# Optimization experiments

Measured on AMD Instinct MI355X. Metric: run time of the kernel, lower is better.

Reference implementation:

```python
import jax, jax.numpy as jnp
from jax import lax
import numpy as np

DIM = 768
HEADS = 12
HD = DIM // HEADS  # 64
STRIDE = (1, 2, 2)
KER = (3, 3, 3)
PAD = [(1, 1), (1, 1), (1, 1)]
EPS = 1e-5


def _layernorm(x, g, b):
    mu = jnp.mean(x, axis=-1, keepdims=True)
    var = jnp.var(x, axis=-1, keepdims=True)
    return (x - mu) * lax.rsqrt(var + EPS) * g + b


def _attention_pool(t, wconv, g, b, T, H, W):
    # t: [B, heads, 1 + T*H*W, HD]; depthwise conv3d pooling on non-cls tokens
    B, Nh, _, Cd = t.shape
    cls_tok = t[:, :, :1, :]
    body = t[:, :, 1:, :].reshape(B * Nh, T, H, W, Cd).transpose(0, 4, 1, 2, 3)  # [BN, C, T, H, W]
    body = lax.conv_general_dilated(
        body, wconv, window_strides=STRIDE, padding=PAD,
        feature_group_count=Cd,
        dimension_numbers=('NCDHW', 'OIDHW', 'NCDHW'))
    Tp, Hp, Wp = body.shape[2], body.shape[3], body.shape[4]
    body = body.reshape(B, Nh, Cd, Tp * Hp * Wp).transpose(0, 1, 3, 2)  # [B, heads, Lp, C]
    t = jnp.concatenate([cls_tok, body], axis=2)
    t = _layernorm(t, g, b)
    return t, (Tp, Hp, Wp)


def setup_inputs() -> dict:
    key = jax.random.key(0)
    ks = jax.random.split(key, 12)
    T, H, W = 8, 28, 28
    B = 4
    N = 1 + T * H * W  # cls + thw tokens = 6273
    s = 0.02
    inp = {
        'x': jax.random.normal(ks[0], (B, N, DIM), jnp.float32),
        'qkv_w': jax.random.normal(ks[1], (DIM, 3 * DIM), jnp.float32) * s,
        'qkv_b': jnp.zeros((3 * DIM,), jnp.float32),
        'proj_w': jax.random.normal(ks[2], (DIM, DIM), jnp.float32) * s,
        'proj_b': jnp.zeros((DIM,), jnp.float32),
        'wq': jax.random.normal(ks[3], (HD, 1, 3, 3, 3), jnp.float32) * s,
        'wk': jax.random.normal(ks[4], (HD, 1, 3, 3, 3), jnp.float32) * s,
        'wv': jax.random.normal(ks[5], (HD, 1, 3, 3, 3), jnp.float32) * s,
        'gq': jnp.ones((HD,), jnp.float32), 'bq': jnp.zeros((HD,), jnp.float32),
        'gk': jnp.ones((HD,), jnp.float32), 'bk': jnp.zeros((HD,), jnp.float32),
        'gv': jnp.ones((HD,), jnp.float32), 'bv': jnp.zeros((HD,), jnp.float32),
        'thw_t': T, 'thw_h': H, 'thw_w': W,
    }
    return inp


def reference(x, qkv_w, qkv_b, proj_w, proj_b, wq, wk, wv,
              gq, bq, gk, bk, gv, bv, thw_t, thw_h, thw_w):
    B, N, C = x.shape
    scale = HD ** -0.5
    qkv = (x @ qkv_w + qkv_b).reshape(B, N, 3, HEADS, HD).transpose(2, 0, 3, 1, 4)
    q, k, v = qkv[0], qkv[1], qkv[2]  # [B, heads, N, HD]
    q, q_shape = _attention_pool(q, wq, gq, bq, thw_t, thw_h, thw_w)
    k, _ = _attention_pool(k, wk, gk, bk, thw_t, thw_h, thw_w)
    v, _ = _attention_pool(v, wv, gv, bv, thw_t, thw_h, thw_w)
    attn = jax.nn.softmax(jnp.einsum('bhqd,bhkd->bhqk', q, k) * scale, axis=-1)
    Nq = q.shape[2]
    out = jnp.einsum('bhqk,bhkd->bhqd', attn, v).transpose(0, 2, 1, 3).reshape(B, Nq, C)
    out = out @ proj_w + proj_b
    return out
```

## Files before the change

kernel.cpp:

```cpp
#include <hip/hip_runtime.h>
#include <hip/hip_bf16.h>

#define BB      4
#define NTOK    6273
#define NPOOL   1569
#define NPOOLP  1600
#define NHEADS  12
#define TT      8
#define HH      28
#define WW      28
#define HP      14
#define WP      14

typedef __attribute__((ext_vector_type(8))) _Float16 f16x8;
typedef __attribute__((ext_vector_type(4))) float f32x4;
typedef unsigned short u16;

#define AS1(p) ((const __attribute__((address_space(1))) void*)(p))
#define AS3(p) ((__attribute__((address_space(3))) void*)(p))

static __device__ __forceinline__ u16 f2h(float x) {
    union { _Float16 h; u16 u; } c; c.h = (_Float16)x; return c.u;
}
static __device__ __forceinline__ float h2f(u16 u) {
    union { u16 u; _Float16 h; } c; c.u = u; return (float)c.h;
}

__global__ __launch_bounds__(256) void cvt_f32_f16_kernel(
    const float* __restrict__ in, u16* __restrict__ out, int n4)
{
    int i = blockIdx.x * 256 + threadIdx.x;
    const int stride = gridDim.x * 256;
    for (; i < n4; i += stride) {
        const float4 v = ((const float4*)in)[i];
        ushort4 o;
        o.x = f2h(v.x); o.y = f2h(v.y); o.z = f2h(v.z); o.w = f2h(v.w);
        ((ushort4*)out)[i] = o;
    }
}

__global__ __launch_bounds__(256) void transpose_cvt_kernel(
    const float* __restrict__ W, u16* __restrict__ t, int K, int N)
{
    __shared__ float tile[32][33];
    const int n0 = blockIdx.x * 32, k0 = blockIdx.y * 32;
    const int tx = threadIdx.x, ty = threadIdx.y;
    #pragma unroll
    for (int i = 0; i < 4; ++i)
        tile[ty + i * 8][tx] = W[(size_t)(k0 + ty + i * 8) * N + n0 + tx];
    __syncthreads();
    #pragma unroll
    for (int i = 0; i < 4; ++i) {
        const int n = n0 + ty + i * 8;
        t[(size_t)n * K + k0 + tx] = f2h(tile[tx][ty + i * 8]);
    }
}

__global__ __launch_bounds__(256) void wt_transpose_kernel(
    const float* __restrict__ wq, const float* __restrict__ wk,
    const float* __restrict__ wv, u16* __restrict__ wTh)
{
    const int which = blockIdx.x;
    const float* w = (which == 0) ? wq : (which == 1) ? wk : wv;
    u16* o = wTh + which * 27 * 64;
    for (int i = threadIdx.x; i < 27 * 64; i += 256) {
        const int j = i >> 6, d = i & 63;
        o[j * 64 + d] = f2h(w[d * 27 + j]);
    }
}

#define GBK 32
#define GNKT 24

__global__ __launch_bounds__(512, 2) void gemm256_qkv_kernel(
    const u16* __restrict__ Af, const u16* __restrict__ Bt,
    const float* __restrict__ bias, int M,
    u16* __restrict__ o0, u16* __restrict__ o1, u16* __restrict__ o2)
{
    __shared__ __align__(16) u16 AB_s[3][2][256 * GBK];

    const int tid  = threadIdx.x;
    const int lane = tid & 63;
    const int w    = tid >> 6;
    const int wr   = w >> 2, wc = w & 3;

    const int nwg = gridDim.x;
    const int qch = nwg >> 3, rch = nwg & 7;
    const int xcd = blockIdx.x & 7, idx = blockIdx.x >> 3;
    const int wg  = (xcd < rch ? xcd * (qch + 1) : rch * (qch + 1) + (xcd - rch) * qch) + idx;
    const int m0 = (wg / 9) * 256;
    const int nb = wg % 9;
    const int n0 = nb * 256;

    const int ch0 = tid, ch1 = 512 + tid;
    const int r0 = ch0 >> 2, c0 = ((ch0 & 3) ^ (r0 & 3)) << 3;
    const int r1 = ch1 >> 2, c1 = ((ch1 & 3) ^ (r1 & 3)) << 3;
    const u16* pA0 = Af + (size_t)min(m0 + r0, M - 1) * 768 + c0;
    const u16* pA1 = Af + (size_t)min(m0 + r1, M - 1) * 768 + c1;
    const u16* pB0 = Bt + (size_t)(n0 + r0) * 768 + c0;
    const u16* pB1 = Bt + (size_t)(n0 + r1) * 768 + c1;
    const int dst0 = (w * 64) * 8;
    const int dst1 = (512 + w * 64) * 8;

    #define STAGE_A(buf, kk) do { \
        __builtin_amdgcn_global_load_lds(AS1(pA0 + (kk)), AS3(&AB_s[buf][0][dst0]), 16, 0, 0); \
        __builtin_amdgcn_global_load_lds(AS1(pA1 + (kk)), AS3(&AB_s[buf][0][dst1]), 16, 0, 0); \
    } while (0)
    #define STAGE_B(buf, kk) do { \
        __builtin_amdgcn_global_load_lds(AS1(pB0 + (kk)), AS3(&AB_s[buf][1][dst0]), 16, 0, 0); \
        __builtin_amdgcn_global_load_lds(AS1(pB1 + (kk)), AS3(&AB_s[buf][1][dst1]), 16, 0, 0); \
    } while (0)

    STAGE_A(0, 0);  STAGE_B(0, 0);
    STAGE_A(1, GBK); STAGE_B(1, GBK);

    f32x4 acc[8][4] = {};
    const int fr = lane & 15, fq = lane >> 4;
    const int sw8 = (fq ^ (fr & 3)) << 3;

    int bufc = 0;
    for (int t = 0; t < GNKT; ++t) {
        if (t < GNKT - 1) asm volatile("s_waitcnt vmcnt(4)" ::: "memory");
        else              asm volatile("s_waitcnt vmcnt(0)" ::: "memory");
        __builtin_amdgcn_s_barrier();

        const u16* As = &AB_s[bufc][0][0];
        const u16* Bs = &AB_s[bufc][1][0];
        const int bufs = (bufc + 2 >= 3) ? bufc - 1 : bufc + 2;
        const int kk = (t + 2) * GBK;

        if (t < GNKT - 2) STAGE_A(bufs, kk);
        f16x8 a[4], b[4];
        #pragma unroll
        for (int m = 0; m < 4; ++m)
            a[m] = *(const f16x8*)&As[(wr * 128 + m * 16 + fr) * GBK + sw8];
        #pragma unroll
        for (int n = 0; n < 4; ++n)
            b[n] = *(const f16x8*)&Bs[(wc * 64 + n * 16 + fr) * GBK + sw8];
        __builtin_amdgcn_s_setprio(1);
        #pragma unroll
        for (int m = 0; m < 4; ++m)
            #pragma unroll
            for (int n = 0; n < 4; ++n)
                acc[m][n] = __builtin_amdgcn_mfma_f32_16x16x32_f16(a[m], b[n], acc[m][n], 0, 0, 0);
        __builtin_amdgcn_s_setprio(0);
        __builtin_amdgcn_s_barrier();

        if (t < GNKT - 2) STAGE_B(bufs, kk);
        #pragma unroll
        for (int m = 0; m < 4; ++m)
            a[m] = *(const f16x8*)&As[(wr * 128 + (m + 4) * 16 + fr) * GBK + sw8];
        __builtin_amdgcn_s_setprio(1);
        #pragma unroll
        for (int m = 0; m < 4; ++m)
            #pragma unroll
            for (int n = 0; n < 4; ++n)
                acc[m + 4][n] = __builtin_amdgcn_mfma_f32_16x16x32_f16(a[m], b[n], acc[m + 4][n], 0, 0, 0);
        __builtin_amdgcn_s_setprio(0);

        bufc = (bufc + 1 >= 3) ? 0 : bufc + 1;
    }
    #undef STAGE_A
    #undef STAGE_B

    const int s = nb / 3;
    u16* const dsts = (s == 0) ? o0 : (s == 1) ? o1 : o2;
    #pragma unroll
    for (int m = 0; m < 8; ++m) {
        const int growb = m0 + wr * 128 + m * 16 + fq * 4;
        #pragma unroll
        for (int j = 0; j < 4; ++j) {
            const int grow = growb + j;
            if (grow >= M) continue;
            const int bidx = grow / NTOK;
            const int ntok = grow - bidx * NTOK;
            #pragma unroll
            for (int n = 0; n < 4; ++n) {
                const int gcol = n0 + wc * 64 + n * 16 + fr;
                const float v = acc[m][n][j] + bias[gcol];
                const int rem = gcol - s * 768;
                const int h = rem >> 6, d = rem & 63;
                dsts[(size_t)((bidx * NHEADS + h) * NTOK + ntok) * 64 + d] = f2h(v);
            }
        }
    }
}

template<int NBLK, bool QKV, typename OutT>
__global__ __launch_bounds__(512) void gemm_fp16_kernel(
    const u16* __restrict__ Af, const u16* __restrict__ Bt,
    const float* __restrict__ bias, int M,
    OutT* __restrict__ o0, OutT* __restrict__ o1, OutT* __restrict__ o2)
{
    __shared__ __align__(16) u16 A_s[128 * 32];
    __shared__ __align__(16) u16 B_s[128 * 32];

    const int tid  = threadIdx.x;
    const int lane = tid & 63;
    const int w    = tid >> 6;
    const int wr   = w >> 2, wc = w & 3;

    const int nwg = gridDim.x;
    const int qch = nwg >> 3, rch = nwg & 7;
    const int xcd = blockIdx.x & 7, idx = blockIdx.x >> 3;
    const int wg  = (xcd < rch ? xcd * (qch + 1) : rch * (qch + 1) + (xcd - rch) * qch) + idx;
    const int m0 = (wg / NBLK) * 128;
    const int n0 = (wg % NBLK) * 128;

    f32x4 acc[4][2] = {};

    const int srow   = lane >> 2;
    const int sslot  = (lane & 3) ^ ((srow >> 1) & 3);

    for (int kt = 0; kt < 24; ++kt) {
        const int k0 = kt * 32;
        __syncthreads();

        {
            const int rb = w * 16;
            const int ra = min(m0 + rb + srow, M - 1);
            __builtin_amdgcn_global_load_lds(AS1(Af + (size_t)ra * 768 + k0 + sslot * 8),
                                             AS3(&A_s[rb * 32]), 16, 0, 0);
            __builtin_amdgcn_global_load_lds(AS1(Bt + (size_t)(n0 + rb + srow) * 768 + k0 + sslot * 8),
                                             AS3(&B_s[rb * 32]), 16, 0, 0);
        }
        __syncthreads();

        const int fr = lane & 15, fq = lane >> 4;
        const int rslot = (fq ^ ((fr >> 1) & 3)) << 3;
        f16x8 a[4], b[2];
        #pragma unroll
        for (int m = 0; m < 4; ++m)
            a[m] = *(const f16x8*)&A_s[(wr * 64 + m * 16 + fr) * 32 + rslot];
        #pragma unroll
        for (int n = 0; n < 2; ++n)
            b[n] = *(const f16x8*)&B_s[(wc * 32 + n * 16 + fr) * 32 + rslot];

        #pragma unroll
        for (int m = 0; m < 4; ++m)
            #pragma unroll
            for (int n = 0; n < 2; ++n)
                acc[m][n] = __builtin_amdgcn_mfma_f32_16x16x32_f16(a[m], b[n], acc[m][n], 0, 0, 0);
    }

    const int fr = lane & 15, fq = lane >> 4;
    #pragma unroll
    for (int m = 0; m < 4; ++m) {
        const int grow_base = m0 + wr * 64 + m * 16 + fq * 4;
        #pragma unroll
        for (int j = 0; j < 4; ++j) {
            const int grow = grow_base + j;
            if (grow >= M) continue;
            int b = 0, ntok = 0;
            if (QKV) { b = grow / NTOK; ntok = grow - b * NTOK; }
            #pragma unroll
            for (int n = 0; n < 2; ++n) {
                const int gcol = n0 + wc * 32 + n * 16 + fr;
                const float v = acc[m][n][j] + bias[gcol];
                if (QKV) {
                    const int s = gcol / 768;
                    const int rem = gcol - s * 768;
                    const int h = rem >> 6, d = rem & 63;
                    OutT* dst = (s == 0) ? o0 : (s == 1) ? o1 : o2;
                    dst[(size_t)((b * NHEADS + h) * NTOK + ntok) * 64 + d] = (OutT)f2h(v);
                } else {
                    o0[(size_t)grow * (NBLK * 128) + gcol] = (OutT)v;
                }
            }
        }
    }
}

#define PL_PG  50
#define PL_NWG (3 * 48 * PL_PG)
__global__ __launch_bounds__(256) void pool_ln_kernel(
    const u16* __restrict__ qr, const u16* __restrict__ kr, const u16* __restrict__ vr,
    const u16* __restrict__ wTh,
    const float* __restrict__ gq, const float* __restrict__ bq,
    const float* __restrict__ gk, const float* __restrict__ bk,
    const float* __restrict__ gv, const float* __restrict__ bv,
    u16* __restrict__ qph, u16* __restrict__ kph, u16* __restrict__ vpt)
{
    const int wg = (blockIdx.x & 7) * (PL_NWG / 8) + (blockIdx.x >> 3);
    const int which = wg / (48 * PL_PG);
    const int rem   = wg - which * (48 * PL_PG);
    const int bh    = rem / PL_PG;
    const int pg    = rem - bh * PL_PG;
    const int wv_   = threadIdx.x >> 6;
    const int lane  = threadIdx.x & 63;
    const int tg    = lane >> 3;
    const int d0    = (lane & 7) * 8;

    const int p  = pg * 32 + wv_ * 8 + tg;
    const int pc = min(p, NPOOL - 1);

    const u16*   in  = (which == 0) ? qr : (which == 1) ? kr : vr;
    const u16*   wTb = wTh + which * 27 * 64;
    const float* g   = (which == 0) ? gq : (which == 1) ? gk : gv;
    const float* bb_ = (which == 0) ? bq : (which == 1) ? bk : bv;
    const float qscale = (which == 0) ? 0.125f : 1.0f;

    const size_t inb = (size_t)bh * NTOK * 64;

    float s[8] = {};
    if (pc == 0) {
        const f16x8 t = *(const f16x8*)&in[inb + d0];
        #pragma unroll
        for (int c = 0; c < 8; ++c) s[c] = (float)t[c];
    } else {
        const int idx = pc - 1;
        const int tp = idx / (HP * WP);
        const int r2 = idx - tp * (HP * WP);
        const int hp = r2 / WP;
        const int wp = r2 - hp * WP;

        const f16x8 z8 = (f16x8)(_Float16)0.0f;
        #pragma unroll
        for (int kt = 0; kt < 3; ++kt) {
            const int it = tp + kt - 1;
            #pragma unroll
            for (int kh = 0; kh < 3; ++kh) {
                const int ih = hp * 2 + kh - 1;
                #pragma unroll
                for (int kw = 0; kw < 3; ++kw) {
                    const int iw = wp * 2 + kw - 1;
                    const int j  = kt * 9 + kh * 3 + kw;
                    const bool ok = (it >= 0) & (it < TT) & (ih >= 0) & (ih < HH) &
                                    (iw >= 0) & (iw < WW);
                    const int n   = 1 + (it * HH + ih) * WW + iw;
                    const int n_c = ok ? n : 0;
                    const f16x8 tv  = *(const f16x8*)&in[inb + (size_t)n_c * 64 + d0];
                    const f16x8 wv8 = *(const f16x8*)&wTb[j * 64 + d0];
                    const f16x8 ts  = ok ? tv : z8;
                    #pragma unroll
                    for (int c = 0; c < 8; ++c)
                        s[c] = fmaf((float)wv8[c], (float)ts[c], s[c]);
                }
            }
        }
    }

    float sum = 0.f, ssq = 0.f;
    #pragma unroll
    for (int c = 0; c < 8; ++c) { sum += s[c]; ssq += s[c] * s[c]; }
    #pragma unroll
    for (int off = 1; off < 8; off <<= 1) {
        sum += __shfl_xor(sum, off);
        ssq += __shfl_xor(ssq, off);
    }
    const float mu  = sum * (1.f / 64.f);
    const float var = ssq * (1.f / 64.f) - mu * mu;
    const float rs  = rsqrtf(var + 1e-5f);

    float g8[8], b8[8];
    {
        const float4 g0 = *(const float4*)&g[d0];
        const float4 g1 = *(const float4*)&g[d0 + 4];
        const float4 b0 = *(const float4*)&bb_[d0];
        const float4 b1 = *(const float4*)&bb_[d0 + 4];
        g8[0]=g0.x; g8[1]=g0.y; g8[2]=g0.z; g8[3]=g0.w;
        g8[4]=g1.x; g8[5]=g1.y; g8[6]=g1.z; g8[7]=g1.w;
        b8[0]=b0.x; b8[1]=b0.y; b8[2]=b0.z; b8[3]=b0.w;
        b8[4]=b1.x; b8[5]=b1.y; b8[6]=b1.z; b8[7]=b1.w;
    }

    u16 oo[8];
    #pragma unroll
    for (int c = 0; c < 8; ++c)
        oo[c] = f2h(((s[c] - mu) * rs * g8[c] + b8[c]) * qscale);

    if (which == 2) {
        u16* base = vpt + (size_t)bh * 64 * NPOOLP + p;
        if (p < NPOOL) {
            #pragma unroll
            for (int c = 0; c < 8; ++c)
                base[(size_t)(d0 + c) * NPOOLP] = oo[c];
        } else {
            #pragma unroll
            for (int c = 0; c < 8; ++c)
                base[(size_t)(d0 + c) * NPOOLP] = 0;
        }
    } else if (p < NPOOL) {
        u16* out = (which == 0) ? qph : kph;
        u16* dst = &out[((size_t)bh * NPOOL + p) * 64 + d0];
        *(ushort4*)&dst[0] = *(ushort4*)&oo[0];
        *(ushort4*)&dst[4] = *(ushort4*)&oo[4];
    }
}

__global__ __launch_bounds__(256) void flash_attn_fp16_kernel(
    const u16* __restrict__ qh, const u16* __restrict__ kh,
    const u16* __restrict__ vt, float* __restrict__ accf,
    float* __restrict__ lf)
{
    __shared__ __align__(16) u16 K_s[64 * 64];
    __shared__ __align__(16) u16 V_s[64 * 64];
    __shared__ __align__(16) u16 P_s[4][32 * 64];

    const int bh = blockIdx.y;
    const int q0 = blockIdx.x * 128;
    const int z  = blockIdx.z;
    const int kt_lo = z ? 13 : 0, kt_hi = z ? 25 : 13;
    const int tid = threadIdx.x;
    const int w = tid >> 6, lane = tid & 63;
    const int fr = lane & 15, fq = lane >> 4;
    const int l8 = lane >> 3;
    const int sw = 8 * ((lane & 7) ^ l8);

    const size_t hb  = (size_t)bh * NPOOL * 64;
    const size_t vtb = (size_t)bh * 64 * NPOOLP;
    float* accb = accf + (size_t)z * BB * NPOOL * 768;
    float* lb   = lf   + (size_t)z * 48 * NPOOL;

    f16x8 qf_[2][2];
    #pragma unroll
    for (int qf = 0; qf < 2; ++qf) {
        const int row = min(q0 + w * 32 + qf * 16 + fr, NPOOL - 1);
        #pragma unroll
        for (int half = 0; half < 2; ++half)
            qf_[qf][half] = *(const f16x8*)&qh[hb + (size_t)row * 64 + half * 32 + fq * 8];
    }

    f16x8 ones;
    #pragma unroll
    for (int i = 0; i < 8; ++i) ones[i] = (_Float16)1.0f;

    f32x4 acc[2][4] = {};
    f32x4 l_acc[2] = {};

    #define LDSW(buf, row, colbyte) \
        (*(const f16x8*)((const char*)(buf) + ((row) * 128 + ((colbyte) ^ (((row) & 7) << 4)))))

    for (int kt = kt_lo; kt < kt_hi; ++kt) {
        const int k0 = kt * 64;
        __syncthreads();

        #pragma unroll
        for (int i = 0; i < 2; ++i) {
            const int rb = w * 16 + i * 8;
            const int r  = rb + l8;
            const int gk = min(k0 + r, NPOOL - 1);
            __builtin_amdgcn_global_load_lds(AS1(kh + hb + (size_t)gk * 64 + sw),
                                             AS3(&K_s[rb * 64]), 16, 0, 0);
            __builtin_amdgcn_global_load_lds(AS1(vt + vtb + (size_t)r * NPOOLP + k0 + sw),
                                             AS3(&V_s[rb * 64]), 16, 0, 0);
        }
        __syncthreads();

        f32x4 sv[2][4];
        #pragma unroll
        for (int nf = 0; nf < 4; ++nf) {
            const int krow = nf * 16 + fr;
            const f16x8 kf0 = LDSW(K_s, krow, fq * 16);
            const f16x8 kf1 = LDSW(K_s, krow, 64 + fq * 16);
            #pragma unroll
            for (int qf = 0; qf < 2; ++qf) {
                f32x4 s = {};
                s = __builtin_amdgcn_mfma_f32_16x16x32_f16(qf_[qf][0], kf0, s, 0, 0, 0);
                s = __builtin_amdgcn_mfma_f32_16x16x32_f16(qf_[qf][1], kf1, s, 0, 0, 0);
                sv[qf][nf] = s;
            }
        }

        #pragma unroll
        for (int nf = 0; nf < 4; ++nf) {
            const bool valid = (k0 + nf * 16 + fr) < NPOOL;
            #pragma unroll
            for (int qf = 0; qf < 2; ++qf) {
                #pragma unroll
                for (int j = 0; j < 4; ++j) {
                    const float p = valid ? __expf(sv[qf][nf][j]) : 0.f;
                    const int row = qf * 16 + fq * 4 + j;
                    const int bo  = row * 128 + ((nf * 32 + fr * 2) ^ ((row & 7) << 4));
                    *(u16*)((char*)&P_s[w][0] + bo) = f2h(p);
                }
            }
        }
        __builtin_amdgcn_sched_barrier(0);

        f16x8 pa[2][2];
        #pragma unroll
        for (int qf = 0; qf < 2; ++qf) {
            const int prow = qf * 16 + fr;
            pa[qf][0] = LDSW(&P_s[w][0], prow, fq * 16);
            pa[qf][1] = LDSW(&P_s[w][0], prow, 64 + fq * 16);
            l_acc[qf] = __builtin_amdgcn_mfma_f32_16x16x32_f16(pa[qf][0], ones, l_acc[qf], 0, 0, 0);
            l_acc[qf] = __builtin_amdgcn_mfma_f32_16x16x32_f16(pa[qf][1], ones, l_acc[qf], 0, 0, 0);
        }
        #pragma unroll
        for (int df = 0; df < 4; ++df) {
            const int vrow = df * 16 + fr;
            const f16x8 v0 = LDSW(V_s, vrow, fq * 16);
            const f16x8 v1 = LDSW(V_s, vrow, 64 + fq * 16);
            acc[0][df] = __builtin_amdgcn_mfma_f32_16x16x32_f16(pa[0][0], v0, acc[0][df], 0, 0, 0);
            acc[0][df] = __builtin_amdgcn_mfma_f32_16x16x32_f16(pa[0][1], v1, acc[0][df], 0, 0, 0);
            acc[1][df] = __builtin_amdgcn_mfma_f32_16x16x32_f16(pa[1][0], v0, acc[1][df], 0, 0, 0);
            acc[1][df] = __builtin_amdgcn_mfma_f32_16x16x32_f16(pa[1][1], v1, acc[1][df], 0, 0, 0);
        }
    }
    #undef LDSW

    const int b = bh / NHEADS, h = bh % NHEADS;
    #pragma unroll
    for (int qf = 0; qf < 2; ++qf) {
        #pragma unroll
        for (int j = 0; j < 4; ++j) {
            const int q = q0 + w * 32 + qf * 16 + fq * 4 + j;
            if (q >= NPOOL) continue;
            float* dst = &accb[((size_t)b * NPOOL + q) * 768 + h * 64];
            #pragma unroll
            for (int df = 0; df < 4; ++df)
                dst[df * 16 + fr] = acc[qf][df][j];
            if (fr == 0)
                lb[(size_t)bh * NPOOL + q] = l_acc[qf][j];
        }
    }
}

__global__ __launch_bounds__(256) void combine_kernel(
    const float* __restrict__ acc0, const float* __restrict__ acc1,
    const float* __restrict__ l0, const float* __restrict__ l1,
    u16* __restrict__ aoh)
{
    const int n4 = BB * NPOOL * 768 / 4;
    int i = blockIdx.x * 256 + threadIdx.x;
    const int stride = gridDim.x * 256;
    for (; i < n4; i += stride) {
        const int e0  = i * 4;
        const int row = e0 / 768;
        const int c   = e0 - row * 768;
        const int b   = row / NPOOL;
        const int q   = row - b * NPOOL;
        const int h   = c >> 6;
        const size_t li = (size_t)(b * NHEADS + h) * NPOOL + q;
        const float inv = 1.f / (l0[li] + l1[li]);
        const float4 a0 = ((const float4*)acc0)[i];
        const float4 a1 = ((const float4*)acc1)[i];
        ushort4 o;
        o.x = f2h((a0.x + a1.x) * inv);
        o.y = f2h((a0.y + a1.y) * inv);
        o.z = f2h((a0.z + a1.z) * inv);
        o.w = f2h((a0.w + a1.w) * inv);
        ((ushort4*)aoh)[i] = o;
    }
}

extern "C" void kernel_launch(void* const* d_in, const int* in_sizes, int n_in,
                              void* d_out, int out_size, void* d_ws, size_t ws_size,
                              hipStream_t stream)
{
    const float* x      = (const float*)d_in[0];
    const float* qkv_w  = (const float*)d_in[1];
    const float* qkv_b  = (const float*)d_in[2];
    const float* proj_w = (const float*)d_in[3];
    const float* proj_b = (const float*)d_in[4];
    const float* wq     = (const float*)d_in[5];
    const float* wk     = (const float*)d_in[6];
    const float* wv     = (const float*)d_in[7];
    const float* gq     = (const float*)d_in[8];
    const float* bq     = (const float*)d_in[9];
    const float* gk     = (const float*)d_in[10];
    const float* bk     = (const float*)d_in[11];
    const float* gv     = (const float*)d_in[12];
    const float* bv     = (const float*)d_in[13];

    const size_t RAW  = (size_t)BB * NHEADS * NTOK * 64;
    const size_t PLD  = (size_t)BB * NHEADS * NPOOL * 64;
    const size_t VTSZ = (size_t)BB * NHEADS * 64 * NPOOLP;
    const size_t AOSZ = (size_t)BB * NPOOL * 768;

    u16* q_raw = (u16*)d_ws;
    u16* k_raw = q_raw + RAW;
    u16* v_raw = k_raw + RAW;
    u16* xh    = v_raw + RAW;
    u16* qph   = xh + RAW;
    u16* kph   = qph + PLD;
    u16* vpb   = kph + PLD;
    u16* vpt   = vpb + PLD;
    u16* wth   = vpt + VTSZ;
    u16* pwth  = wth + (size_t)2304 * 768;
    u16* wTh   = pwth + (size_t)768 * 768;
    float* acc0 = (float*)(wTh + 3 * 27 * 64);
    float* acc1 = acc0 + AOSZ;
    float* l0   = acc1 + AOSZ;
    float* l1   = l0 + (size_t)48 * NPOOL;
    u16* aoh   = q_raw;

    cvt_f32_f16_kernel<<<2048, 256, 0, stream>>>(x, xh, (int)(RAW / 4));

    transpose_cvt_kernel<<<dim3(2304 / 32, 768 / 32), dim3(32, 8), 0, stream>>>(
        qkv_w, wth, 768, 2304);
    transpose_cvt_kernel<<<dim3(768 / 32, 768 / 32), dim3(32, 8), 0, stream>>>(
        proj_w, pwth, 768, 768);
    wt_transpose_kernel<<<3, 256, 0, stream>>>(wq, wk, wv, wTh);

    gemm256_qkv_kernel<<<dim3(99 * 9), 512, 0, stream>>>(
        xh, wth, qkv_b, BB * NTOK, q_raw, k_raw, v_raw);

    pool_ln_kernel<<<dim3(PL_NWG), 256, 0, stream>>>(
        q_raw, k_raw, v_raw, wTh, gq, bq, gk, bk, gv, bv,
        qph, kph, vpt);

    flash_attn_fp16_kernel<<<dim3(13, 48, 2), 256, 0, stream>>>(
        qph, kph, vpt, acc0, l0);

    combine_kernel<<<2048, 256, 0, stream>>>(acc0, acc1, l0, l1, aoh);

    gemm_fp16_kernel<6, false, float><<<dim3(50 * 6), 512, 0, stream>>>(
        aoh, pwth, proj_b, BB * NPOOL, (float*)d_out, nullptr, nullptr);
}
```

Measured before the change: 324.6 us.

## Restructure QKV GEMM to BK=64 with 8 half-tile LDS slots and quadrant pipeline

New measurement: 319.9 us. About the same (-1.4%).

```diff
diff --git a/kernel.cpp b/kernel.cpp
--- a/kernel.cpp
+++ b/kernel.cpp
@@ -69,20 +69,22 @@
     }
 }
 
-#define GBK 32
-#define GNKT 24
+#define GBK 64
+#define GNKT 12
 
 __global__ __launch_bounds__(512, 2) void gemm256_qkv_kernel(
     const u16* __restrict__ Af, const u16* __restrict__ Bt,
     const float* __restrict__ bias, int M,
     u16* __restrict__ o0, u16* __restrict__ o1, u16* __restrict__ o2)
 {
-    __shared__ __align__(16) u16 AB_s[3][2][256 * GBK];
+    __shared__ __align__(16) u16 A_s[4][128 * 64];
+    __shared__ __align__(16) u16 B_s[4][128 * 64];
 
     const int tid  = threadIdx.x;
     const int lane = tid & 63;
     const int w    = tid >> 6;
-    const int wr   = w >> 2, wc = w & 3;
+    const int wr   = w >> 2;
+    const int wc   = w & 3;
 
     const int nwg = gridDim.x;
     const int qch = nwg >> 3, rch = nwg & 7;
@@ -92,76 +94,119 @@
     const int nb = wg % 9;
     const int n0 = nb * 256;
 
-    const int ch0 = tid, ch1 = 512 + tid;
-    const int r0 = ch0 >> 2, c0 = ((ch0 & 3) ^ (r0 & 3)) << 3;
-    const int r1 = ch1 >> 2, c1 = ((ch1 & 3) ^ (r1 & 3)) << 3;
-    const u16* pA0 = Af + (size_t)min(m0 + r0, M - 1) * 768 + c0;
-    const u16* pA1 = Af + (size_t)min(m0 + r1, M - 1) * 768 + c1;
-    const u16* pB0 = Bt + (size_t)(n0 + r0) * 768 + c0;
-    const u16* pB1 = Bt + (size_t)(n0 + r1) * 768 + c1;
-    const int dst0 = (w * 64) * 8;
-    const int dst1 = (512 + w * 64) * 8;
-
-    #define STAGE_A(buf, kk) do { \
-        __builtin_amdgcn_global_load_lds(AS1(pA0 + (kk)), AS3(&AB_s[buf][0][dst0]), 16, 0, 0); \
-        __builtin_amdgcn_global_load_lds(AS1(pA1 + (kk)), AS3(&AB_s[buf][0][dst1]), 16, 0, 0); \
-    } while (0)
-    #define STAGE_B(buf, kk) do { \
-        __builtin_amdgcn_global_load_lds(AS1(pB0 + (kk)), AS3(&AB_s[buf][1][dst0]), 16, 0, 0); \
-        __builtin_amdgcn_global_load_lds(AS1(pB1 + (kk)), AS3(&AB_s[buf][1][dst1]), 16, 0, 0); \
-    } while (0)
-
-    STAGE_A(0, 0);  STAGE_B(0, 0);
-    STAGE_A(1, GBK); STAGE_B(1, GBK);
+    const int srow = tid >> 3;
+    const int scc  = ((tid & 7) ^ (srow & 7)) * 8;
+    unsigned offA[2][2], offB[2][2];
+    #pragma unroll
+    for (int h = 0; h < 2; ++h)
+        #pragma unroll
+        for (int i = 0; i < 2; ++i) {
+            offA[h][i] = (unsigned)(min(m0 + h * 128 + i * 64 + srow, M - 1) * 768 + scc);
+            offB[h][i] = (unsigned)((n0 + h * 128 + i * 64 + srow) * 768 + scc);
+        }
+
+#define STGA(slot, h, tt) do { \
+    __builtin_amdgcn_global_load_lds(AS1(Af + offA[h][0] + (tt) * 64), AS3(&A_s[slot][w * 512]), 16, 0, 0); \
+    __builtin_amdgcn_global_load_lds(AS1(Af + offA[h][1] + (tt) * 64), AS3(&A_s[slot][4096 + w * 512]), 16, 0, 0); \
+} while (0)
+#define STGB(slot, h, tt) do { \
+    __builtin_amdgcn_global_load_lds(AS1(Bt + offB[h][0] + (tt) * 64), AS3(&B_s[slot][w * 512]), 16, 0, 0); \
+    __builtin_amdgcn_global_load_lds(AS1(Bt + offB[h][1] + (tt) * 64), AS3(&B_s[slot][4096 + w * 512]), 16, 0, 0); \
+} while (0)
+
+    STGA(0, 0, 0); STGB(0, 0, 0); STGA(1, 1, 0); STGB(1, 1, 0);
+    STGA(2, 0, 1); STGB(2, 0, 1); STGA(3, 1, 1);
+    asm volatile("s_waitcnt vmcnt(6)" ::: "memory");
+    __builtin_amdgcn_s_barrier();
 
     f32x4 acc[8][4] = {};
     const int fr = lane & 15, fq = lane >> 4;
-    const int sw8 = (fq ^ (fr & 3)) << 3;
-
-    int bufc = 0;
-    for (int t = 0; t < GNKT; ++t) {
-        if (t < GNKT - 1) asm volatile("s_waitcnt vmcnt(4)" ::: "memory");
-        else              asm volatile("s_waitcnt vmcnt(0)" ::: "memory");
-        __builtin_amdgcn_s_barrier();
-
-        const u16* As = &AB_s[bufc][0][0];
-        const u16* Bs = &AB_s[bufc][1][0];
-        const int bufs = (bufc + 2 >= 3) ? bufc - 1 : bufc + 2;
-        const int kk = (t + 2) * GBK;
-
-        if (t < GNKT - 2) STAGE_A(bufs, kk);
-        f16x8 a[4], b[4];
-        #pragma unroll
-        for (int m = 0; m < 4; ++m)
-            a[m] = *(const f16x8*)&As[(wr * 128 + m * 16 + fr) * GBK + sw8];
-        #pragma unroll
-        for (int n = 0; n < 4; ++n)
-            b[n] = *(const f16x8*)&Bs[(wc * 64 + n * 16 + fr) * GBK + sw8];
-        __builtin_amdgcn_s_setprio(1);
-        #pragma unroll
-        for (int m = 0; m < 4; ++m)
-            #pragma unroll
-            for (int n = 0; n < 4; ++n)
-                acc[m][n] = __builtin_amdgcn_mfma_f32_16x16x32_f16(a[m], b[n], acc[m][n], 0, 0, 0);
-        __builtin_amdgcn_s_setprio(0);
-        __builtin_amdgcn_s_barrier();
-
-        if (t < GNKT - 2) STAGE_B(bufs, kk);
-        #pragma unroll
-        for (int m = 0; m < 4; ++m)
-            a[m] = *(const f16x8*)&As[(wr * 128 + (m + 4) * 16 + fr) * GBK + sw8];
-        __builtin_amdgcn_s_setprio(1);
-        #pragma unroll
-        for (int m = 0; m < 4; ++m)
-            #pragma unroll
-            for (int n = 0; n < 4; ++n)
-                acc[m + 4][n] = __builtin_amdgcn_mfma_f32_16x16x32_f16(a[m], b[n], acc[m + 4][n], 0, 0, 0);
-        __builtin_amdgcn_s_setprio(0);
-
-        bufc = (bufc + 1 >= 3) ? 0 : bufc + 1;
-    }
-    #undef STAGE_A
-    #undef STAGE_B
+    const int ck0 = (fq ^ (fr & 7)) * 8;
+    const int ck1 = ((4 + fq) ^ (fr & 7)) * 8;
+    const int arow = fr * 64;
+    const int brow = (wc & 1) * 4096 + fr * 64;
+
+    for (int it = 0; it < GNKT / 2; ++it) {
+        #pragma unroll
+        for (int par = 0; par < 2; ++par) {
+            const int t  = it * 2 + par;
+            const int sa = par ? 2 + wr : wr;
+            const int sb = par ? 2 + (wc >> 1) : (wc >> 1);
+
+            f16x8 aF[4][2], aG[4][2], bLo[2][2], bHi[2][2];
+
+            if (t < GNKT - 1) STGB(par ? 1 : 3, 1, t + 1);
+            #pragma unroll
+            for (int m = 0; m < 4; ++m)
+                #pragma unroll
+                for (int kh = 0; kh < 2; ++kh)
+                    aF[m][kh] = *(const f16x8*)&A_s[sa][m * 1024 + arow + (kh ? ck1 : ck0)];
+            #pragma unroll
+            for (int n = 0; n < 2; ++n)
+                #pragma unroll
+                for (int kh = 0; kh < 2; ++kh)
+                    bLo[n][kh] = *(const f16x8*)&B_s[sb][brow + n * 1024 + (kh ? ck1 : ck0)];
+            __builtin_amdgcn_s_setprio(1);
+            #pragma unroll
+            for (int m = 0; m < 4; ++m)
+                #pragma unroll
+                for (int n = 0; n < 2; ++n) {
+                    acc[m][n] = __builtin_amdgcn_mfma_f32_16x16x32_f16(aF[m][0], bLo[n][0], acc[m][n], 0, 0, 0);
+                    acc[m][n] = __builtin_amdgcn_mfma_f32_16x16x32_f16(aF[m][1], bLo[n][1], acc[m][n], 0, 0, 0);
+                }
+            __builtin_amdgcn_s_setprio(0);
+            __builtin_amdgcn_s_barrier();
+
+            #pragma unroll
+            for (int n = 0; n < 2; ++n)
+                #pragma unroll
+                for (int kh = 0; kh < 2; ++kh)
+                    bHi[n][kh] = *(const f16x8*)&B_s[sb][brow + (n + 2) * 1024 + (kh ? ck1 : ck0)];
+            __builtin_amdgcn_s_setprio(1);
+            #pragma unroll
+            for (int m = 0; m < 4; ++m)
+                #pragma unroll
+                for (int n = 0; n < 2; ++n) {
+                    acc[m][n + 2] = __builtin_amdgcn_mfma_f32_16x16x32_f16(aF[m][0], bHi[n][0], acc[m][n + 2], 0, 0, 0);
+                    acc[m][n + 2] = __builtin_amdgcn_mfma_f32_16x16x32_f16(aF[m][1], bHi[n][1], acc[m][n + 2], 0, 0, 0);
+                }
+            __builtin_amdgcn_s_setprio(0);
+            __builtin_amdgcn_s_barrier();
+
+            if (t < GNKT - 2) STGB(par ? 2 : 0, 0, t + 2);
+            #pragma unroll
+            for (int m = 0; m < 4; ++m)
+                #pragma unroll
+                for (int kh = 0; kh < 2; ++kh)
+                    aG[m][kh] = *(const f16x8*)&A_s[sa][(m + 4) * 1024 + arow + (kh ? ck1 : ck0)];
+            __builtin_amdgcn_s_setprio(1);
+            #pragma unroll
+            for (int m = 0; m < 4; ++m)
+                #pragma unroll
+                for (int n = 0; n < 2; ++n) {
+                    acc[m + 4][n + 2] = __builtin_amdgcn_mfma_f32_16x16x32_f16(aG[m][0], bHi[n][0], acc[m + 4][n + 2], 0, 0, 0);
+                    acc[m + 4][n + 2] = __builtin_amdgcn_mfma_f32_16x16x32_f16(aG[m][1], bHi[n][1], acc[m + 4][n + 2], 0, 0, 0);
+                }
+            __builtin_amdgcn_s_setprio(0);
+            __builtin_amdgcn_s_barrier();
+
+            if (t < GNKT - 2) { STGA(par ? 2 : 0, 0, t + 2); STGA(par ? 3 : 1, 1, t + 2); }
+            __builtin_amdgcn_s_setprio(1);
+            #pragma unroll
+            for (int m = 0; m < 4; ++m)
+                #pragma unroll
+                for (int n = 0; n < 2; ++n) {
+                    acc[m + 4][n] = __builtin_amdgcn_mfma_f32_16x16x32_f16(aG[m][0], bLo[n][0], acc[m + 4][n], 0, 0, 0);
+                    acc[m + 4][n] = __builtin_amdgcn_mfma_f32_16x16x32_f16(aG[m][1], bLo[n][1], acc[m + 4][n], 0, 0, 0);
+                }
+            __builtin_amdgcn_s_setprio(0);
+            if (t < GNKT - 2) asm volatile("s_waitcnt vmcnt(6)" ::: "memory");
+            else              asm volatile("s_waitcnt vmcnt(0)" ::: "memory");
+            __builtin_amdgcn_s_barrier();
+        }
+    }
+#undef STGA
+#undef STGB
 
     const int s = nb / 3;
     u16* const dsts = (s == 0) ? o0 : (s == 1) ? o1 : o2;
```
